# Optimization experiments

Measured on AMD Instinct MI355X. Metric: run time of the kernel, lower is better.

The kernel has to match this reference:

```python
import jax, jax.numpy as jnp
import numpy as np

N_NODES = 50000
N_EDGES = 800000
N_GRAPHS = 64
IN_CH = 128
EMB = 64


def gcn_conv(x, W, b, src, dst, w, n):
    """PyG GCNConv: add self-loops (weight 1), symmetric normalization,
    linear transform, scatter-sum aggregation, bias."""
    loop = jnp.arange(n, dtype=src.dtype)
    src2 = jnp.concatenate([src, loop])
    dst2 = jnp.concatenate([dst, loop])
    w2 = jnp.concatenate([w, jnp.ones((n,), dtype=x.dtype)])
    deg = jax.ops.segment_sum(w2, dst2, num_segments=n)
    dinv = jnp.where(deg > 0, jax.lax.rsqrt(jnp.where(deg > 0, deg, 1.0)), 0.0)
    norm = dinv[src2] * w2 * dinv[dst2]  # [E+N]
    h = x @ W  # [N, out]
    msg = norm[:, None] * h[src2]  # [E+N, out]
    return jax.ops.segment_sum(msg, dst2, num_segments=n) + b


def setup_inputs() -> dict:
    key = jax.random.key(0)
    ks = jax.random.split(key, 16)
    x = jax.random.normal(ks[0], (N_NODES, IN_CH), dtype=jnp.float32)
    edge_index = jax.random.randint(ks[1], (2, N_EDGES), 0, N_NODES, dtype=jnp.int32)
    edge_attr = jax.random.uniform(ks[2], (N_EDGES,), dtype=jnp.float32)
    batch_index = jnp.sort(jax.random.randint(ks[3], (N_NODES,), 0, N_GRAPHS, dtype=jnp.int32))
    def glorot(k, shape):
        lim = float(np.sqrt(6.0 / (shape[0] + shape[1])))
        return jax.random.uniform(k, shape, dtype=jnp.float32, minval=-lim, maxval=lim)
    return {
        "x": x, "edge_index": edge_index, "edge_attr": edge_attr, "batch_index": batch_index,
        "W0": glorot(ks[4], (IN_CH, EMB)), "b0": jnp.zeros((EMB,), jnp.float32),
        "W1": glorot(ks[5], (EMB, EMB)), "b1": jnp.zeros((EMB,), jnp.float32),
        "W2": glorot(ks[6], (EMB, EMB)), "b2": jnp.zeros((EMB,), jnp.float32),
        "W3": glorot(ks[7], (EMB, EMB)), "b3": jnp.zeros((EMB,), jnp.float32),
        "Wout": glorot(ks[8], (2 * EMB, 1)), "bout": jnp.zeros((1,), jnp.float32),
    }


def reference(x, edge_index, edge_attr, batch_index, W0, b0, W1, b1, W2, b2, W3, b3, Wout, bout):
    n = x.shape[0]
    src, dst = edge_index[0], edge_index[1]
    h = jnp.tanh(gcn_conv(x, W0, b0, src, dst, edge_attr, n))
    h = jnp.tanh(gcn_conv(h, W1, b1, src, dst, edge_attr, n))
    h = jnp.tanh(gcn_conv(h, W2, b2, src, dst, edge_attr, n))
    h = jnp.tanh(gcn_conv(h, W3, b3, src, dst, edge_attr, n))
    gmax = jax.ops.segment_max(h, batch_index, num_segments=N_GRAPHS)
    gsum = jax.ops.segment_sum(h, batch_index, num_segments=N_GRAPHS)
    cnt = jax.ops.segment_sum(jnp.ones((n,), h.dtype), batch_index, num_segments=N_GRAPHS)
    gmean = gsum / jnp.maximum(cnt, 1.0)[:, None]
    pooled = jnp.concatenate([gmax, gmean], axis=1)  # [B, 2*EMB]
    return (pooled @ Wout + bout).reshape(-1)
```

## Files before the change

kernel.cpp:

```cpp
#include <hip/hip_runtime.h>
#include <hip/hip_fp16.h>
#include <math.h>
#include <limits.h>

#define N_NODES 50000
#define N_EDGES 800000
#define N_GRAPHS 64
#define IN_CH 128
#define EMB 64
#define POOL_CHUNK 16
#define CPAD 32

__global__ void init_k(int* counts, int* total, int* gmax, float* gsum, int* cnt) {
    int i = blockIdx.x * blockDim.x + threadIdx.x;
    if (i < N_NODES * CPAD) counts[i] = 0;
    if (i == 0) *total = 0;
    if (i < N_GRAPHS * EMB) { gmax[i] = INT_MIN; gsum[i] = 0.f; }
    if (i < N_GRAPHS) cnt[i] = 0;
}

__global__ void hist_k(const int* __restrict__ dst, int* counts,
                       int* __restrict__ slot_in) {
    int e = blockIdx.x * blockDim.x + threadIdx.x;
    if (e >= N_EDGES) return;
    slot_in[e] = atomicAdd(&counts[(size_t)dst[e] * CPAD], 1);
}

__global__ void alloc_k(const int* __restrict__ counts, int* __restrict__ row_start,
                        int* __restrict__ row_end, int* total) {
    int i = blockIdx.x * blockDim.x + threadIdx.x;
    int lane = threadIdx.x & 63;
    int c = (i < N_NODES) ? counts[(size_t)i * CPAD] : 0;
    int inc = c;
    for (int off = 1; off < 64; off <<= 1) {
        int v = __shfl_up(inc, off);
        if (lane >= off) inc += v;
    }
    int base;
    if (lane == 63) base = atomicAdd(total, inc);
    base = __shfl(base, 63);
    int excl = base + inc - c;
    if (i < N_NODES) { row_start[i] = excl; row_end[i] = excl + c; }
}

__global__ void scatter_k(const int* __restrict__ src, const int* __restrict__ dst,
                          const float* __restrict__ w, const int* __restrict__ slot_in,
                          const int* __restrict__ row_start, int2* __restrict__ csr) {
    int e = blockIdx.x * blockDim.x + threadIdx.x;
    if (e >= N_EDGES) return;
    int d = dst[e];
    int slot = row_start[d] + slot_in[e];
    csr[slot] = make_int2(src[e], __float_as_int(w[e]));
}

__global__ __launch_bounds__(256) void deg_dinv_k(const int2* __restrict__ csr,
                                                  const int* __restrict__ row_start,
                                                  const int* __restrict__ row_end,
                                                  float* __restrict__ dinv) {
    int node = (blockIdx.x * blockDim.x + threadIdx.x) >> 6;
    int lane = threadIdx.x & 63;
    if (node >= N_NODES) return;
    int beg = row_start[node], end = row_end[node];
    float s = 0.f;
    for (int i = beg + lane; i < end; i += 64) s += __int_as_float(csr[i].y);
    for (int off = 32; off > 0; off >>= 1) s += __shfl_down(s, off);
    if (lane == 0) {
        float d = 1.0f + s;
        dinv[node] = d > 0.f ? rsqrtf(d) : 0.f;
    }
}

__global__ __launch_bounds__(256) void normfix_k(int2* __restrict__ csr,
                                                 const int* __restrict__ row_start,
                                                 const int* __restrict__ row_end,
                                                 const float* __restrict__ dinv) {
    int node = (blockIdx.x * blockDim.x + threadIdx.x) >> 6;
    int lane = threadIdx.x & 63;
    if (node >= N_NODES) return;
    int beg = row_start[node], end = row_end[node];
    float dd = dinv[node];
    for (int i = beg + lane; i < end; i += 64) {
        int2 r = csr[i];
        float nm = dinv[r.x] * __int_as_float(r.y) * dd;
        csr[i] = make_int2(r.x, __float_as_int(nm));
    }
}

template<int K>
__global__ __launch_bounds__(256) void gemm_k(const float* __restrict__ A,
                                              const float* __restrict__ W,
                                              __half* __restrict__ out) {
    __shared__ float Al[64 * K];
    __shared__ float Wl[K * EMB];
    int tid = threadIdx.x;
    long rowBase = (long)blockIdx.x * 64;
    int validRows = (int)min((long)64, (long)N_NODES - rowBase);

    const float4* Ag = (const float4*)(A + rowBase * K);
    for (int i = tid; i < validRows * (K / 4); i += 256) {
        int r = i / (K / 4), kc = i % (K / 4);
        float4 v = Ag[(long)r * (K / 4) + kc];
        *(float4*)&Al[r * K + 4 * (kc ^ (r & 3))] = v;
    }
    const float4* Wg = (const float4*)W;
    float4* Wl4 = (float4*)Wl;
    for (int i = tid; i < K * EMB / 4; i += 256) Wl4[i] = Wg[i];
    __syncthreads();

    int tc = tid & 15, tr = tid >> 4;
    int r0 = tr * 4, c0 = tc * 4;
    float acc[4][4] = {};
#pragma unroll 2
    for (int k = 0; k < K; k += 4) {
        int kc = k >> 2;
        float4 a[4], w[4];
#pragma unroll
        for (int i = 0; i < 4; ++i)
            a[i] = *(const float4*)&Al[(r0 + i) * K + 4 * (kc ^ i)];
#pragma unroll
        for (int j = 0; j < 4; ++j)
            w[j] = *(const float4*)&Wl[(k + j) * EMB + c0];
#pragma unroll
        for (int i = 0; i < 4; ++i) {
            const float* ai = (const float*)&a[i];
#pragma unroll
            for (int kk = 0; kk < 4; ++kk) {
                float av = ai[kk];
                const float* wk = (const float*)&w[kk];
#pragma unroll
                for (int j = 0; j < 4; ++j) acc[i][j] += av * wk[j];
            }
        }
    }
#pragma unroll
    for (int i = 0; i < 4; ++i) {
        long row = rowBase + r0 + i;
        if (row < N_NODES) {
            __half2 p0 = __floats2half2_rn(acc[i][0], acc[i][1]);
            __half2 p1 = __floats2half2_rn(acc[i][2], acc[i][3]);
            uint2 u = make_uint2(*(unsigned int*)&p0, *(unsigned int*)&p1);
            *(uint2*)&out[row * EMB + c0] = u;
        }
    }
}

__global__ __launch_bounds__(256) void fused_agg_k(const __half* __restrict__ h,
                                                   const int2* __restrict__ csr,
                                                   const int* __restrict__ row_start,
                                                   const int* __restrict__ row_end,
                                                   const float* __restrict__ dinv,
                                                   const float* __restrict__ b,
                                                   float* __restrict__ out) {
    int node = (blockIdx.x * blockDim.x + threadIdx.x) >> 6;
    int lane = threadIdx.x & 63;
    if (node >= N_NODES) return;
    float di = dinv[node];
    float acc = di * di * __half2float(h[(long)node * EMB + lane]) + b[lane];
    int e = row_start[node];
    int end = row_end[node];
    for (; e + 7 < end; e += 8) {
        int2 r[8];
        __half v[8];
#pragma unroll
        for (int i = 0; i < 8; ++i) r[i] = csr[e + i];
#pragma unroll
        for (int i = 0; i < 8; ++i) v[i] = h[(long)r[i].x * EMB + lane];
#pragma unroll
        for (int i = 0; i < 8; ++i) acc += __int_as_float(r[i].y) * __half2float(v[i]);
    }
    for (; e + 3 < end; e += 4) {
        int2 r0 = csr[e], r1 = csr[e + 1], r2 = csr[e + 2], r3 = csr[e + 3];
        float v0 = __half2float(h[(long)r0.x * EMB + lane]);
        float v1 = __half2float(h[(long)r1.x * EMB + lane]);
        float v2 = __half2float(h[(long)r2.x * EMB + lane]);
        float v3 = __half2float(h[(long)r3.x * EMB + lane]);
        acc += __int_as_float(r0.y) * v0;
        acc += __int_as_float(r1.y) * v1;
        acc += __int_as_float(r2.y) * v2;
        acc += __int_as_float(r3.y) * v3;
    }
    for (; e < end; ++e) {
        int2 r0 = csr[e];
        acc += __int_as_float(r0.y) * __half2float(h[(long)r0.x * EMB + lane]);
    }
    __builtin_nontemporal_store(tanhf(acc), &out[(long)node * EMB + lane]);
}

__device__ inline int f2ord(float x) {
    int bb = __float_as_int(x);
    return bb >= 0 ? bb : (bb ^ 0x7fffffff);
}
__device__ inline float ord2f(int k) {
    return __int_as_float(k >= 0 ? k : (k ^ 0x7fffffff));
}

__global__ __launch_bounds__(256) void pool_k(const float* __restrict__ h,
                                              const int* __restrict__ batch,
                                              int* gmax, float* gsum, int* cnt) {
    int wave = (blockIdx.x * blockDim.x + threadIdx.x) >> 6;
    int lane = threadIdx.x & 63;
    int start = wave * POOL_CHUNK;
    if (start >= N_NODES) return;
    int bsel = (lane < POOL_CHUNK) ? batch[start + lane] : 0;
    float v[POOL_CHUNK];
#pragma unroll
    for (int i = 0; i < POOL_CHUNK; ++i)
        v[i] = h[(long)(start + i) * EMB + lane];
    int curg = __shfl(bsel, 0);
    float mx = -INFINITY, sm = 0.f;
    int ct = 0;
#pragma unroll
    for (int i = 0; i < POOL_CHUNK; ++i) {
        int g = __shfl(bsel, i);
        if (g != curg) {
            atomicMax(&gmax[curg * EMB + lane], f2ord(mx));
            atomicAdd(&gsum[curg * EMB + lane], sm);
            if (lane == 0) atomicAdd(&cnt[curg], ct);
            curg = g; mx = -INFINITY; sm = 0.f; ct = 0;
        }
        mx = fmaxf(mx, v[i]);
        sm += v[i];
        ++ct;
    }
    atomicMax(&gmax[curg * EMB + lane], f2ord(mx));
    atomicAdd(&gsum[curg * EMB + lane], sm);
    if (lane == 0) atomicAdd(&cnt[curg], ct);
}

__global__ void final_k(const int* __restrict__ gmax, const float* __restrict__ gsum,
                        const int* __restrict__ cnt, const float* __restrict__ Wout,
                        const float* __restrict__ bout, float* __restrict__ out) {
    int g = threadIdx.x;
    if (g >= N_GRAPHS) return;
    float c = fmaxf((float)cnt[g], 1.0f);
    float acc = bout[0];
    for (int ch = 0; ch < EMB; ++ch) {
        acc += ord2f(gmax[g * EMB + ch]) * Wout[ch]
             + (gsum[g * EMB + ch] / c) * Wout[EMB + ch];
    }
    out[g] = acc;
}

extern "C" void kernel_launch(void* const* d_in, const int* in_sizes, int n_in,
                              void* d_out, int out_size, void* d_ws, size_t ws_size,
                              hipStream_t stream) {
    const float* x         = (const float*)d_in[0];
    const int*   edge_idx  = (const int*)d_in[1];
    const float* edge_attr = (const float*)d_in[2];
    const int*   batch     = (const int*)d_in[3];
    const float* W0 = (const float*)d_in[4];
    const float* b0 = (const float*)d_in[5];
    const float* W1 = (const float*)d_in[6];
    const float* b1 = (const float*)d_in[7];
    const float* W2 = (const float*)d_in[8];
    const float* b2 = (const float*)d_in[9];
    const float* W3 = (const float*)d_in[10];
    const float* b3 = (const float*)d_in[11];
    const float* Wout = (const float*)d_in[12];
    const float* bout = (const float*)d_in[13];
    float* out = (float*)d_out;

    const int* src = edge_idx;
    const int* dst = edge_idx + N_EDGES;

    char* ws = (char*)d_ws;
    float*  dinv      = (float*)ws;  ws += (size_t)N_NODES * sizeof(float);
    int*    counts    = (int*)ws;    ws += (size_t)N_NODES * CPAD * sizeof(int);
    int*    row_start = (int*)ws;    ws += (size_t)N_NODES * sizeof(int);
    int*    row_end   = (int*)ws;    ws += (size_t)N_NODES * sizeof(int);
    int*    slot_in   = (int*)ws;    ws += (size_t)N_EDGES * sizeof(int);
    int*    total     = (int*)ws;    ws += 4 * sizeof(int);
    int2*   csr       = (int2*)ws;   ws += (size_t)N_EDGES * sizeof(int2);
    __half* bufL      = (__half*)ws; ws += (size_t)N_NODES * EMB * sizeof(__half);
    float*  bufH      = (float*)ws;  ws += (size_t)N_NODES * EMB * sizeof(float);
    int*    gmax      = (int*)ws;    ws += N_GRAPHS * EMB * sizeof(int);
    float*  gsum      = (float*)ws;  ws += N_GRAPHS * EMB * sizeof(float);
    int*    cnt       = (int*)ws;    ws += N_GRAPHS * sizeof(int);

    const int nodeB = (N_NODES + 255) / 256;
    const int edgeB = (N_EDGES + 255) / 256;
    const int waveB = (N_NODES * 64 + 255) / 256;
    const int gemmB = (N_NODES + 63) / 64;
    const int initB = (N_NODES * CPAD + 255) / 256;

    init_k<<<initB, 256, 0, stream>>>(counts, total, gmax, gsum, cnt);
    hist_k<<<edgeB, 256, 0, stream>>>(dst, counts, slot_in);
    alloc_k<<<nodeB, 256, 0, stream>>>(counts, row_start, row_end, total);
    scatter_k<<<edgeB, 256, 0, stream>>>(src, dst, edge_attr, slot_in, row_start, csr);
    deg_dinv_k<<<waveB, 256, 0, stream>>>(csr, row_start, row_end, dinv);
    normfix_k<<<waveB, 256, 0, stream>>>(csr, row_start, row_end, dinv);

    const float* Wl[4] = {W0, W1, W2, W3};
    const float* bl[4] = {b0, b1, b2, b3};
    for (int l = 0; l < 4; ++l) {
        if (l == 0) gemm_k<IN_CH><<<gemmB, 256, 0, stream>>>(x, Wl[0], bufL);
        else        gemm_k<EMB>  <<<gemmB, 256, 0, stream>>>(bufH, Wl[l], bufL);
        fused_agg_k<<<waveB, 256, 0, stream>>>(bufL, csr, row_start, row_end, dinv, bl[l], bufH);
    }

    pool_k<<<(((N_NODES + POOL_CHUNK - 1) / POOL_CHUNK) * 64 + 255) / 256, 256, 0, stream>>>(
        bufH, batch, gmax, gsum, cnt);
    final_k<<<1, 64, 0, stream>>>(gmax, gsum, cnt, Wout, bout, out);
}
```

Measured before the change: 382.7 us.

## Fold GCN normalization into GEMM/agg epilogues, compute degree in histogram, store activations in fp16

Edge-weight degree sums are now accumulated with float atomics during the histogram pass and dinv is computed in the allocation kernel. This removes the separate degree and norm-fix passes over the CSR. The symmetric normalization is refactored: the GEMM pre-scales rows by dinv[src] and the aggregation post-scales by dinv[dst], so edges use the raw weight. Layer outputs are stored as fp16 to halve activation traffic. This adds float atomic contention on counts, nondeterministic summation order, and fp16 precision loss on activations.

```diff
diff --git a/kernel.cpp b/kernel.cpp
--- a/kernel.cpp
+++ b/kernel.cpp
@@ -19,15 +19,17 @@
     if (i < N_GRAPHS) cnt[i] = 0;
 }
 
-__global__ void hist_k(const int* __restrict__ dst, int* counts,
-                       int* __restrict__ slot_in) {
+__global__ void hist_k(const int* __restrict__ dst, const float* __restrict__ w,
+                       int* counts, int* __restrict__ slot_in) {
     int e = blockIdx.x * blockDim.x + threadIdx.x;
     if (e >= N_EDGES) return;
-    slot_in[e] = atomicAdd(&counts[(size_t)dst[e] * CPAD], 1);
+    size_t base = (size_t)dst[e] * CPAD;
+    slot_in[e] = atomicAdd(&counts[base], 1);
+    atomicAdd((float*)&counts[base + 1], w[e]);
 }
 
 __global__ void alloc_k(const int* __restrict__ counts, int* __restrict__ row_start,
-                        int* __restrict__ row_end, int* total) {
+                        int* __restrict__ row_end, int* total, float* __restrict__ dinv) {
     int i = blockIdx.x * blockDim.x + threadIdx.x;
     int lane = threadIdx.x & 63;
     int c = (i < N_NODES) ? counts[(size_t)i * CPAD] : 0;
@@ -40,7 +42,12 @@
     if (lane == 63) base = atomicAdd(total, inc);
     base = __shfl(base, 63);
     int excl = base + inc - c;
-    if (i < N_NODES) { row_start[i] = excl; row_end[i] = excl + c; }
+    if (i < N_NODES) {
+        row_start[i] = excl;
+        row_end[i] = excl + c;
+        float d = 1.0f + __int_as_float(counts[(size_t)i * CPAD + 1]);
+        dinv[i] = d > 0.f ? rsqrtf(d) : 0.f;
+    }
 }
 
 __global__ void scatter_k(const int* __restrict__ src, const int* __restrict__ dst,
@@ -53,42 +60,10 @@
     csr[slot] = make_int2(src[e], __float_as_int(w[e]));
 }
 
-__global__ __launch_bounds__(256) void deg_dinv_k(const int2* __restrict__ csr,
-                                                  const int* __restrict__ row_start,
-                                                  const int* __restrict__ row_end,
-                                                  float* __restrict__ dinv) {
-    int node = (blockIdx.x * blockDim.x + threadIdx.x) >> 6;
-    int lane = threadIdx.x & 63;
-    if (node >= N_NODES) return;
-    int beg = row_start[node], end = row_end[node];
-    float s = 0.f;
-    for (int i = beg + lane; i < end; i += 64) s += __int_as_float(csr[i].y);
-    for (int off = 32; off > 0; off >>= 1) s += __shfl_down(s, off);
-    if (lane == 0) {
-        float d = 1.0f + s;
-        dinv[node] = d > 0.f ? rsqrtf(d) : 0.f;
-    }
-}
-
-__global__ __launch_bounds__(256) void normfix_k(int2* __restrict__ csr,
-                                                 const int* __restrict__ row_start,
-                                                 const int* __restrict__ row_end,
-                                                 const float* __restrict__ dinv) {
-    int node = (blockIdx.x * blockDim.x + threadIdx.x) >> 6;
-    int lane = threadIdx.x & 63;
-    if (node >= N_NODES) return;
-    int beg = row_start[node], end = row_end[node];
-    float dd = dinv[node];
-    for (int i = beg + lane; i < end; i += 64) {
-        int2 r = csr[i];
-        float nm = dinv[r.x] * __int_as_float(r.y) * dd;
-        csr[i] = make_int2(r.x, __float_as_int(nm));
-    }
-}
-
-template<int K>
-__global__ __launch_bounds__(256) void gemm_k(const float* __restrict__ A,
+template<int K, bool HALF_IN>
+__global__ __launch_bounds__(256) void gemm_k(const void* __restrict__ A_,
                                               const float* __restrict__ W,
+                                              const float* __restrict__ dinv,
                                               __half* __restrict__ out) {
     __shared__ float Al[64 * K];
     __shared__ float Wl[K * EMB];
@@ -96,11 +71,22 @@
     long rowBase = (long)blockIdx.x * 64;
     int validRows = (int)min((long)64, (long)N_NODES - rowBase);
 
-    const float4* Ag = (const float4*)(A + rowBase * K);
-    for (int i = tid; i < validRows * (K / 4); i += 256) {
-        int r = i / (K / 4), kc = i % (K / 4);
-        float4 v = Ag[(long)r * (K / 4) + kc];
-        *(float4*)&Al[r * K + 4 * (kc ^ (r & 3))] = v;
+    if constexpr (HALF_IN) {
+        const __half* Ah = (const __half*)A_ + rowBase * K;
+        for (int i = tid; i < validRows * (K / 4); i += 256) {
+            int r = i / (K / 4), kc = i % (K / 4);
+            const __half2* p = (const __half2*)(Ah + (long)r * K + 4 * kc);
+            float2 lo = __half22float2(p[0]);
+            float2 hi = __half22float2(p[1]);
+            *(float4*)&Al[r * K + 4 * (kc ^ (r & 3))] = make_float4(lo.x, lo.y, hi.x, hi.y);
+        }
+    } else {
+        const float4* Ag = (const float4*)((const float*)A_ + rowBase * K);
+        for (int i = tid; i < validRows * (K / 4); i += 256) {
+            int r = i / (K / 4), kc = i % (K / 4);
+            float4 v = Ag[(long)r * (K / 4) + kc];
+            *(float4*)&Al[r * K + 4 * (kc ^ (r & 3))] = v;
+        }
     }
     const float4* Wg = (const float4*)W;
     float4* Wl4 = (float4*)Wl;
@@ -136,26 +122,27 @@
     for (int i = 0; i < 4; ++i) {
         long row = rowBase + r0 + i;
         if (row < N_NODES) {
-            __half2 p0 = __floats2half2_rn(acc[i][0], acc[i][1]);
-            __half2 p1 = __floats2half2_rn(acc[i][2], acc[i][3]);
+            float dv = dinv[row];
+            __half2 p0 = __floats2half2_rn(dv * acc[i][0], dv * acc[i][1]);
+            __half2 p1 = __floats2half2_rn(dv * acc[i][2], dv * acc[i][3]);
             uint2 u = make_uint2(*(unsigned int*)&p0, *(unsigned int*)&p1);
             *(uint2*)&out[row * EMB + c0] = u;
         }
     }
 }
 
-__global__ __launch_bounds__(256) void fused_agg_k(const __half* __restrict__ h,
+__global__ __launch_bounds__(256) void fused_agg_k(const __half* __restrict__ hs,
                                                    const int2* __restrict__ csr,
                                                    const int* __restrict__ row_start,
                                                    const int* __restrict__ row_end,
                                                    const float* __restrict__ dinv,
                                                    const float* __restrict__ b,
-                                                   float* __restrict__ out) {
+                                                   __half* __restrict__ out) {
     int node = (blockIdx.x * blockDim.x + threadIdx.x) >> 6;
     int lane = threadIdx.x & 63;
     if (node >= N_NODES) return;
     float di = dinv[node];
-    float acc = di * di * __half2float(h[(long)node * EMB + lane]) + b[lane];
+    float acc = __half2float(hs[(long)node * EMB + lane]);
     int e = row_start[node];
     int end = row_end[node];
     for (; e + 7 < end; e += 8) {
@@ -164,16 +151,16 @@
 #pragma unroll
         for (int i = 0; i < 8; ++i) r[i] = csr[e + i];
 #pragma unroll
-        for (int i = 0; i < 8; ++i) v[i] = h[(long)r[i].x * EMB + lane];
+        for (int i = 0; i < 8; ++i) v[i] = hs[(long)r[i].x * EMB + lane];
 #pragma unroll
         for (int i = 0; i < 8; ++i) acc += __int_as_float(r[i].y) * __half2float(v[i]);
     }
     for (; e + 3 < end; e += 4) {
         int2 r0 = csr[e], r1 = csr[e + 1], r2 = csr[e + 2], r3 = csr[e + 3];
-        float v0 = __half2float(h[(long)r0.x * EMB + lane]);
-        float v1 = __half2float(h[(long)r1.x * EMB + lane]);
-        float v2 = __half2float(h[(long)r2.x * EMB + lane]);
-        float v3 = __half2float(h[(long)r3.x * EMB + lane]);
+        float v0 = __half2float(hs[(long)r0.x * EMB + lane]);
+        float v1 = __half2float(hs[(long)r1.x * EMB + lane]);
+        float v2 = __half2float(hs[(long)r2.x * EMB + lane]);
+        float v3 = __half2float(hs[(long)r3.x * EMB + lane]);
         acc += __int_as_float(r0.y) * v0;
         acc += __int_as_float(r1.y) * v1;
         acc += __int_as_float(r2.y) * v2;
@@ -181,9 +168,12 @@
     }
     for (; e < end; ++e) {
         int2 r0 = csr[e];
-        acc += __int_as_float(r0.y) * __half2float(h[(long)r0.x * EMB + lane]);
-    }
-    __builtin_nontemporal_store(tanhf(acc), &out[(long)node * EMB + lane]);
+        acc += __int_as_float(r0.y) * __half2float(hs[(long)r0.x * EMB + lane]);
+    }
+    float o = tanhf(di * acc + b[lane]);
+    __half oh = __float2half(o);
+    __builtin_nontemporal_store(*(unsigned short*)&oh,
+                                (unsigned short*)&out[(long)node * EMB + lane]);
 }
 
 __device__ inline int f2ord(float x) {
@@ -194,7 +184,7 @@
     return __int_as_float(k >= 0 ? k : (k ^ 0x7fffffff));
 }
 
-__global__ __launch_bounds__(256) void pool_k(const float* __restrict__ h,
+__global__ __launch_bounds__(256) void pool_k(const __half* __restrict__ h,
                                               const int* __restrict__ batch,
                                               int* gmax, float* gsum, int* cnt) {
     int wave = (blockIdx.x * blockDim.x + threadIdx.x) >> 6;
@@ -205,7 +195,7 @@
     float v[POOL_CHUNK];
 #pragma unroll
     for (int i = 0; i < POOL_CHUNK; ++i)
-        v[i] = h[(long)(start + i) * EMB + lane];
+        v[i] = __half2float(h[(long)(start + i) * EMB + lane]);
     int curg = __shfl(bsel, 0);
     float mx = -INFINITY, sm = 0.f;
     int ct = 0;
@@ -272,7 +262,7 @@
     int*    total     = (int*)ws;    ws += 4 * sizeof(int);
     int2*   csr       = (int2*)ws;   ws += (size_t)N_EDGES * sizeof(int2);
     __half* bufL      = (__half*)ws; ws += (size_t)N_NODES * EMB * sizeof(__half);
-    float*  bufH      = (float*)ws;  ws += (size_t)N_NODES * EMB * sizeof(float);
+    __half* bufH      = (__half*)ws; ws += (size_t)N_NODES * EMB * sizeof(__half);
     int*    gmax      = (int*)ws;    ws += N_GRAPHS * EMB * sizeof(int);
     float*  gsum      = (float*)ws;  ws += N_GRAPHS * EMB * sizeof(float);
     int*    cnt       = (int*)ws;    ws += N_GRAPHS * sizeof(int);
@@ -284,17 +274,15 @@
     const int initB = (N_NODES * CPAD + 255) / 256;
 
     init_k<<<initB, 256, 0, stream>>>(counts, total, gmax, gsum, cnt);
-    hist_k<<<edgeB, 256, 0, stream>>>(dst, counts, slot_in);
-    alloc_k<<<nodeB, 256, 0, stream>>>(counts, row_start, row_end, total);
+    hist_k<<<edgeB, 256, 0, stream>>>(dst, edge_attr, counts, slot_in);
+    alloc_k<<<nodeB, 256, 0, stream>>>(counts, row_start, row_end, total, dinv);
     scatter_k<<<edgeB, 256, 0, stream>>>(src, dst, edge_attr, slot_in, row_start, csr);
-    deg_dinv_k<<<waveB, 256, 0, stream>>>(csr, row_start, row_end, dinv);
-    normfix_k<<<waveB, 256, 0, stream>>>(csr, row_start, row_end, dinv);
 
     const float* Wl[4] = {W0, W1, W2, W3};
     const float* bl[4] = {b0, b1, b2, b3};
     for (int l = 0; l < 4; ++l) {
-        if (l == 0) gemm_k<IN_CH><<<gemmB, 256, 0, stream>>>(x, Wl[0], bufL);
-        else        gemm_k<EMB>  <<<gemmB, 256, 0, stream>>>(bufH, Wl[l], bufL);
+        if (l == 0) gemm_k<IN_CH, false><<<gemmB, 256, 0, stream>>>(x, Wl[0], dinv, bufL);
+        else        gemm_k<EMB, true>   <<<gemmB, 256, 0, stream>>>(bufH, Wl[l], dinv, bufL);
         fused_agg_k<<<waveB, 256, 0, stream>>>(bufL, csr, row_start, row_end, dinv, bl[l], bufH);
     }
 
```

After: 415.2 us. +8.5%, slower.
